# Performance work log

Hardware: AMD Instinct MI355X
Metric: run time of the kernel (lower is better)

Reference implementation:

```python
import jax, jax.numpy as jnp
import numpy as np

N_NODES = 100000
N_EDGES = 1600000
NEG_SLOPE = 0.01  # F.leaky_relu default


def _param(key, shape, scale=0.05):
    return jax.random.normal(key, shape, dtype=jnp.float32) * scale


def setup_inputs() -> dict:
    key = jax.random.key(0)
    ks = jax.random.split(key, 32)
    inp = {
        "x": jax.random.normal(ks[0], (N_NODES, 64), dtype=jnp.float32),
        "edge_index": jax.random.randint(ks[1], (2, N_EDGES), 0, N_NODES, dtype=jnp.int64),
        # encoder SAGEConv params: lin_l (neighbors, with bias) + lin_r (root)
        "ggn1_Wl": _param(ks[2], (128, 64)), "ggn1_b": jnp.zeros((128,), jnp.float32), "ggn1_Wr": _param(ks[3], (128, 64)),
        "ggn2_Wl": _param(ks[4], (128, 128)), "ggn2_b": jnp.zeros((128,), jnp.float32), "ggn2_Wr": _param(ks[5], (128, 128)),
        "ggn3_Wl": _param(ks[6], (128, 128)), "ggn3_b": jnp.zeros((128,), jnp.float32), "ggn3_Wr": _param(ks[7], (128, 128)),
        "tr2_W": _param(ks[8], (64, 128)), "tr2_b": jnp.zeros((64,), jnp.float32),
        # decoder
        "dec1_W": _param(ks[9], (128, 64)), "dec1_b": jnp.zeros((128,), jnp.float32),
        "dec2_Wl": _param(ks[10], (128, 128)), "dec2_b": jnp.zeros((128,), jnp.float32), "dec2_Wr": _param(ks[11], (128, 128)),
        "dec3_Wl": _param(ks[12], (64, 128)), "dec3_b": jnp.zeros((64,), jnp.float32), "dec3_Wr": _param(ks[13], (64, 128)),
        "dec4_Wl": _param(ks[14], (3, 64)), "dec4_b": jnp.zeros((3,), jnp.float32), "dec4_Wr": _param(ks[15], (3, 64)),
    }
    return inp


def _sage(x, src, dst, Wl, b, Wr, n):
    # PyG SAGEConv (aggr='mean'): lin_l(mean_{j->i} x_j) + lin_r(x_i)
    msgs = x[src]                                              # [E, d] gather
    s = jax.ops.segment_sum(msgs, dst, num_segments=n)          # [N, d]
    cnt = jax.ops.segment_sum(jnp.ones((src.shape[0], 1), x.dtype), dst, num_segments=n)
    mean = s / jnp.maximum(cnt, 1.0)
    return mean @ Wl.T + b + x @ Wr.T


def _leaky(h):
    return jnp.where(h > 0, h, NEG_SLOPE * h)


def reference(x, edge_index,
              ggn1_Wl, ggn1_b, ggn1_Wr,
              ggn2_Wl, ggn2_b, ggn2_Wr,
              ggn3_Wl, ggn3_b, ggn3_Wr,
              tr2_W, tr2_b,
              dec1_W, dec1_b,
              dec2_Wl, dec2_b, dec2_Wr,
              dec3_Wl, dec3_b, dec3_Wr,
              dec4_Wl, dec4_b, dec4_Wr):
    n = x.shape[0]
    src, dst = edge_index[0], edge_index[1]  # source_to_target flow
    # --- encode (dropout = identity, deterministic reference) ---
    h = jnp.tanh(_sage(x, src, dst, ggn1_Wl, ggn1_b, ggn1_Wr, n))
    h = jnp.tanh(_sage(h, src, dst, ggn2_Wl, ggn2_b, ggn2_Wr, n))
    h = jnp.tanh(_sage(h, src, dst, ggn3_Wl, ggn3_b, ggn3_Wr, n))
    mu = h @ tr2_W.T + tr2_b
    logvar = mu  # module applies the same tr2 twice
    z = mu       # reparametrize in eval mode returns mu
    # --- decode ---
    o = _leaky(z @ dec1_W.T + dec1_b)
    o = _leaky(_sage(o, src, dst, dec2_Wl, dec2_b, dec2_Wr, n))
    o = jnp.tanh(_sage(o, src, dst, dec3_Wl, dec3_b, dec3_Wr, n))
    z2 = _sage(o, src, dst, dec4_Wl, dec4_b, dec4_Wr, n)
    return (z2[:, :2], z2[:, 2], mu, logvar)
```

## Files before the change

### kernel.cpp

```cpp
#include <hip/hip_runtime.h>
#include <cmath>


constexpr int ACT_NONE = 0, ACT_TANH = 1, ACT_LEAKY = 2;
constexpr int SCAN_CHUNK = 4096;

typedef __attribute__((ext_vector_type(8))) __bf16 bf16x8;
typedef __attribute__((ext_vector_type(4))) float f32x4;
typedef __attribute__((ext_vector_type(4))) unsigned short u16x4;

__device__ __forceinline__ unsigned short f2h(float x) {
  _Float16 h = (_Float16)x;
  unsigned short u;
  __builtin_memcpy(&u, &h, 2);
  return u;
}
__device__ __forceinline__ float hlo(unsigned int u) {
  unsigned short s = (unsigned short)(u & 0xffffu);
  _Float16 h;
  __builtin_memcpy(&h, &s, 2);
  return (float)h;
}
__device__ __forceinline__ float hhi(unsigned int u) {
  unsigned short s = (unsigned short)(u >> 16);
  _Float16 h;
  __builtin_memcpy(&h, &s, 2);
  return (float)h;
}
__device__ __forceinline__ void split_bf16(float x, __bf16& h, __bf16& l) {
  h = (__bf16)x;
  l = (__bf16)(x - (float)h);
}
__device__ __forceinline__ unsigned short b2u(__bf16 b) {
  unsigned short u;
  __builtin_memcpy(&u, &b, 2);
  return u;
}

__global__ __launch_bounds__(256) void split_x_kernel(const float* __restrict__ in,
                                                      __bf16* __restrict__ hi,
                                                      __bf16* __restrict__ lo, int total) {
  int i = (blockIdx.x * 256 + threadIdx.x) * 4;
  if (i >= total) return;
  float4 v = *(const float4*)(in + i);
  float vv[4] = {v.x, v.y, v.z, v.w};
  u16x4 h, l;
#pragma unroll
  for (int j = 0; j < 4; ++j) {
    __bf16 hb, lb;
    split_bf16(vv[j], hb, lb);
    h[j] = b2u(hb);
    l[j] = b2u(lb);
  }
  *(u16x4*)(hi + i) = h;
  *(u16x4*)(lo + i) = l;
}

__global__ __launch_bounds__(256) void split_w_kernel(
    const float* p0, const float* p1, const float* p2, const float* p3,
    const float* p4, const float* p5, const float* p6, const float* p7,
    const float* p8, const float* p9, const float* p10, const float* p11,
    __bf16* __restrict__ hi, __bf16* __restrict__ lo) {
  int b = blockIdx.x;
  const float* src;
  int boff, doff;
  if      (b < 8)   { src = p0;  boff = b;       doff = 0; }
  else if (b < 16)  { src = p1;  boff = b - 8;   doff = 8192; }
  else if (b < 32)  { src = p2;  boff = b - 16;  doff = 16384; }
  else if (b < 48)  { src = p3;  boff = b - 32;  doff = 32768; }
  else if (b < 64)  { src = p4;  boff = b - 48;  doff = 49152; }
  else if (b < 80)  { src = p5;  boff = b - 64;  doff = 65536; }
  else if (b < 88)  { src = p6;  boff = b - 80;  doff = 81920; }
  else if (b < 96)  { src = p7;  boff = b - 88;  doff = 90112; }
  else if (b < 112) { src = p8;  boff = b - 96;  doff = 98304; }
  else if (b < 128) { src = p9;  boff = b - 112; doff = 114688; }
  else if (b < 136) { src = p10; boff = b - 128; doff = 131072; }
  else              { src = p11; boff = b - 136; doff = 139264; }
  int i = boff * 1024 + threadIdx.x * 4;
  float4 v = *(const float4*)(src + i);
  float vv[4] = {v.x, v.y, v.z, v.w};
  u16x4 h, l;
#pragma unroll
  for (int j = 0; j < 4; ++j) {
    __bf16 hb, lb;
    split_bf16(vv[j], hb, lb);
    h[j] = b2u(hb);
    l[j] = b2u(lb);
  }
  *(u16x4*)(hi + doff + i) = h;
  *(u16x4*)(lo + doff + i) = l;
}

__global__ __launch_bounds__(256) void count_rank_kernel(const int* __restrict__ dst,
                                                         int* __restrict__ cnt,
                                                         int* __restrict__ rank, int E) {
  int e = blockIdx.x * 256 + threadIdx.x;
  if (e < E) rank[e] = atomicAdd(&cnt[dst[e]], 1);
}

__global__ __launch_bounds__(1024) void scan_blk_kernel(const int* __restrict__ cnt,
                                                        int* __restrict__ rowptr,
                                                        float* __restrict__ inv,
                                                        int* __restrict__ bsum, int n) {
  __shared__ int wsum[17];
  const int lane = threadIdx.x & 63;
  const int wid = threadIdx.x >> 6;
  const int i0 = blockIdx.x * SCAN_CHUNK + threadIdx.x * 4;
  int v[4];
  if (i0 + 3 < n) {
    int4 t = *(const int4*)(cnt + i0);
    v[0] = t.x; v[1] = t.y; v[2] = t.z; v[3] = t.w;
  } else {
#pragma unroll
    for (int j = 0; j < 4; ++j) v[j] = (i0 + j < n) ? cnt[i0 + j] : 0;
  }
#pragma unroll
  for (int j = 0; j < 4; ++j)
    if (i0 + j < n) inv[i0 + j] = 1.0f / (float)(v[j] > 1 ? v[j] : 1);
  const int s = v[0] + v[1] + v[2] + v[3];
  int x = s;
#pragma unroll
  for (int off = 1; off < 64; off <<= 1) {
    int t = __shfl_up(x, off);
    if (lane >= off) x += t;
  }
  if (lane == 63) wsum[wid + 1] = x;
  __syncthreads();
  if (threadIdx.x == 0) {
    wsum[0] = 0;
    for (int w = 1; w <= 16; ++w) wsum[w] += wsum[w - 1];
    bsum[blockIdx.x] = wsum[16];
  }
  __syncthreads();
  int p = wsum[wid] + x - s;
#pragma unroll
  for (int j = 0; j < 4; ++j) {
    if (i0 + j < n) rowptr[i0 + j] = p;
    p += v[j];
  }
}

__global__ __launch_bounds__(1024) void scan_sums_kernel(int* __restrict__ bsum,
                                                         int* __restrict__ rowptr,
                                                         int nb, int n) {
  __shared__ int wsum[17];
  const int lane = threadIdx.x & 63;
  const int wid = threadIdx.x >> 6;
  const int v = (threadIdx.x < nb) ? bsum[threadIdx.x] : 0;
  int x = v;
#pragma unroll
  for (int off = 1; off < 64; off <<= 1) {
    int t = __shfl_up(x, off);
    if (lane >= off) x += t;
  }
  if (lane == 63) wsum[wid + 1] = x;
  __syncthreads();
  if (threadIdx.x == 0) {
    wsum[0] = 0;
    for (int w = 1; w <= 16; ++w) wsum[w] += wsum[w - 1];
    rowptr[n] = wsum[16];
  }
  __syncthreads();
  if (threadIdx.x < nb) bsum[threadIdx.x] = wsum[wid] + x - v;
}

__global__ __launch_bounds__(1024) void scan_add_kernel(int* __restrict__ rowptr,
                                                        const int* __restrict__ bsum,
                                                        int n) {
  const int off = bsum[blockIdx.x];
  const int i0 = blockIdx.x * SCAN_CHUNK + threadIdx.x * 4;
  if (i0 + 3 < n) {
    int4 t = *(const int4*)(rowptr + i0);
    t.x += off; t.y += off; t.z += off; t.w += off;
    *(int4*)(rowptr + i0) = t;
  } else {
    for (int j = 0; j < 4; ++j)
      if (i0 + j < n) rowptr[i0 + j] += off;
  }
}

__global__ __launch_bounds__(256) void scatter_kernel(const int* __restrict__ src,
                                                      const int* __restrict__ dst,
                                                      const int* __restrict__ rowptr,
                                                      const int* __restrict__ rank,
                                                      int* __restrict__ esrc, int E) {
  int e = blockIdx.x * 256 + threadIdx.x;
  if (e < E) esrc[rowptr[dst[e]] + rank[e]] = src[e];
}

__global__ __launch_bounds__(256) void gather_f32s_kernel(
    const float* __restrict__ in, const int* __restrict__ esrc,
    const int* __restrict__ rowptr, const float* __restrict__ inv,
    __bf16* __restrict__ Mhi, __bf16* __restrict__ Mlo, int n) {
  const int node = blockIdx.x * 4 + (threadIdx.x >> 6);
  const int lane = threadIdx.x & 63;
  if (node >= n) return;
  const int beg = rowptr[node];
  const int end = rowptr[node + 1];
  const float iv = inv[node];
  float a0 = 0.f, a1 = 0.f, a2 = 0.f, a3 = 0.f;
  for (int b = beg; b < end; b += 64) {
    int m = end - b;
    if (m > 64) m = 64;
    int myi = (lane < m) ? esrc[b + lane] : 0;
    int s = 0;
    for (; s + 4 <= m; s += 4) {
      int i0 = __shfl(myi, s);
      int i1 = __shfl(myi, s + 1);
      int i2 = __shfl(myi, s + 2);
      int i3 = __shfl(myi, s + 3);
      a0 += in[(size_t)i0 * 64 + lane];
      a1 += in[(size_t)i1 * 64 + lane];
      a2 += in[(size_t)i2 * 64 + lane];
      a3 += in[(size_t)i3 * 64 + lane];
    }
    for (; s < m; ++s) {
      int i0 = __shfl(myi, s);
      a0 += in[(size_t)i0 * 64 + lane];
    }
  }
  float mv = ((a0 + a1) + (a2 + a3)) * iv;
  __bf16 h, l;
  split_bf16(mv, h, l);
  Mhi[(size_t)node * 64 + lane] = h;
  Mlo[(size_t)node * 64 + lane] = l;
}

__global__ __launch_bounds__(256) void gather_s16_kernel(
    const unsigned short* __restrict__ inq, const int* __restrict__ esrc,
    const int* __restrict__ rowptr, const float* __restrict__ inv,
    __bf16* __restrict__ Mhi, __bf16* __restrict__ Mlo, int n) {
  const int node = blockIdx.x * 4 + (threadIdx.x >> 6);
  const int lane = threadIdx.x & 63;
  if (node >= n) return;
  const int beg = rowptr[node];
  const int end = rowptr[node + 1];
  const float iv = inv[node] * (1.0f / 32767.0f);
  const unsigned int* bu = (const unsigned int*)inq;
  int a0l = 0, a0h = 0, a1l = 0, a1h = 0;
  int a2l = 0, a2h = 0, a3l = 0, a3h = 0;
  for (int b = beg; b < end; b += 64) {
    int m = end - b;
    if (m > 64) m = 64;
    int myi = (lane < m) ? esrc[b + lane] : 0;
    int s = 0;
    for (; s + 4 <= m; s += 4) {
      int i0 = __shfl(myi, s);
      int i1 = __shfl(myi, s + 1);
      int i2 = __shfl(myi, s + 2);
      int i3 = __shfl(myi, s + 3);
      unsigned int u0 = bu[(size_t)i0 * 64 + lane];
      unsigned int u1 = bu[(size_t)i1 * 64 + lane];
      unsigned int u2 = bu[(size_t)i2 * 64 + lane];
      unsigned int u3 = bu[(size_t)i3 * 64 + lane];
      a0l += (int)(short)u0; a0h += ((int)u0) >> 16;
      a1l += (int)(short)u1; a1h += ((int)u1) >> 16;
      a2l += (int)(short)u2; a2h += ((int)u2) >> 16;
      a3l += (int)(short)u3; a3h += ((int)u3) >> 16;
    }
    for (; s < m; ++s) {
      int i0 = __shfl(myi, s);
      unsigned int u0 = bu[(size_t)i0 * 64 + lane];
      a0l += (int)(short)u0; a0h += ((int)u0) >> 16;
    }
  }
  float rx = (float)((a0l + a1l) + (a2l + a3l)) * iv;
  float ry = (float)((a0h + a1h) + (a2h + a3h)) * iv;
  __bf16 h0, l0, h1, l1;
  split_bf16(rx, h0, l0);
  split_bf16(ry, h1, l1);
  ((unsigned int*)Mhi)[(size_t)node * 64 + lane] =
      (unsigned int)b2u(h0) | ((unsigned int)b2u(h1) << 16);
  ((unsigned int*)Mlo)[(size_t)node * 64 + lane] =
      (unsigned int)b2u(l0) | ((unsigned int)b2u(l1) << 16);
}

__global__ __launch_bounds__(256) void gather_h128_kernel(
    const unsigned short* __restrict__ inh, const int* __restrict__ esrc,
    const int* __restrict__ rowptr, const float* __restrict__ inv,
    __bf16* __restrict__ Mhi, __bf16* __restrict__ Mlo, int n) {
  const int node = blockIdx.x * 4 + (threadIdx.x >> 6);
  const int lane = threadIdx.x & 63;
  if (node >= n) return;
  const int beg = rowptr[node];
  const int end = rowptr[node + 1];
  const float iv = inv[node];
  const unsigned int* bu = (const unsigned int*)inh;
  float a0x = 0.f, a0y = 0.f, a1x = 0.f, a1y = 0.f;
  float a2x = 0.f, a2y = 0.f, a3x = 0.f, a3y = 0.f;
  for (int b = beg; b < end; b += 64) {
    int m = end - b;
    if (m > 64) m = 64;
    int myi = (lane < m) ? esrc[b + lane] : 0;
    int s = 0;
    for (; s + 4 <= m; s += 4) {
      int i0 = __shfl(myi, s);
      int i1 = __shfl(myi, s + 1);
      int i2 = __shfl(myi, s + 2);
      int i3 = __shfl(myi, s + 3);
      unsigned int u0 = bu[(size_t)i0 * 64 + lane];
      unsigned int u1 = bu[(size_t)i1 * 64 + lane];
      unsigned int u2 = bu[(size_t)i2 * 64 + lane];
      unsigned int u3 = bu[(size_t)i3 * 64 + lane];
      a0x += hlo(u0); a0y += hhi(u0);
      a1x += hlo(u1); a1y += hhi(u1);
      a2x += hlo(u2); a2y += hhi(u2);
      a3x += hlo(u3); a3y += hhi(u3);
    }
    for (; s < m; ++s) {
      int i0 = __shfl(myi, s);
      unsigned int u0 = bu[(size_t)i0 * 64 + lane];
      a0x += hlo(u0); a0y += hhi(u0);
    }
  }
  float rx = ((a0x + a1x) + (a2x + a3x)) * iv;
  float ry = ((a0y + a1y) + (a2y + a3y)) * iv;
  __bf16 h0, l0, h1, l1;
  split_bf16(rx, h0, l0);
  split_bf16(ry, h1, l1);
  ((unsigned int*)Mhi)[(size_t)node * 64 + lane] =
      (unsigned int)b2u(h0) | ((unsigned int)b2u(h1) << 16);
  ((unsigned int*)Mlo)[(size_t)node * 64 + lane] =
      (unsigned int)b2u(l0) | ((unsigned int)b2u(l1) << 16);
}

__global__ __launch_bounds__(256) void gather_h64_kernel(
    const unsigned short* __restrict__ inh, const int* __restrict__ esrc,
    const int* __restrict__ rowptr, const float* __restrict__ inv,
    float* __restrict__ meanb, int n) {
  const int node = blockIdx.x * 4 + (threadIdx.x >> 6);
  const int lane = threadIdx.x & 63;
  if (node >= n) return;
  const int beg = rowptr[node];
  const int end = rowptr[node + 1];
  const float iv = inv[node];
  const unsigned int* bu = (const unsigned int*)inh;
  const int half = lane >> 5;
  const int hl = lane & 31;
  float ax = 0.f, ay = 0.f, bx = 0.f, by = 0.f;
  for (int b = beg; b < end; b += 64) {
    int m = end - b;
    if (m > 64) m = 64;
    int myi = (lane < m) ? esrc[b + lane] : 0;
    int s = 0;
    for (; s + 4 <= m; s += 4) {
      int i0 = __shfl(myi, s + half);
      int i1 = __shfl(myi, s + 2 + half);
      unsigned int u0 = bu[(size_t)i0 * 32 + hl];
      unsigned int u1 = bu[(size_t)i1 * 32 + hl];
      ax += hlo(u0); ay += hhi(u0);
      bx += hlo(u1); by += hhi(u1);
    }
    for (; s < m; s += 2) {
      int t = s + half;
      if (t < m) {
        int i0 = __shfl(myi, t);
        unsigned int u0 = bu[(size_t)i0 * 32 + hl];
        ax += hlo(u0); ay += hhi(u0);
      }
    }
  }
  float sx = ax + bx, sy = ay + by;
  sx += __shfl_xor(sx, 32);
  sy += __shfl_xor(sy, 32);
  if (half == 0)
    ((float2*)meanb)[(size_t)node * 32 + hl] = make_float2(sx * iv, sy * iv);
}

__global__ __launch_bounds__(256) void gather_mean4_kernel(
    const float* __restrict__ y4, const int* __restrict__ esrc,
    const int* __restrict__ rowptr, const float* __restrict__ inv,
    float* __restrict__ mean4, int n) {
  int i = blockIdx.x * 256 + threadIdx.x;
  if (i >= n) return;
  const int beg = rowptr[i], end = rowptr[i + 1];
  const float iv = inv[i];
  float sx = 0.f, sy = 0.f, sz = 0.f;
  const float4* b = (const float4*)y4;
  for (int j = beg; j < end; ++j) {
    float4 v = b[esrc[j]];
    sx += v.x; sy += v.y; sz += v.z;
  }
  ((float4*)mean4)[i] = make_float4(sx * iv, sy * iv, sz * iv, 0.f);
}

template <int DI, int DO, int ACT, bool AGG, bool ADDMEAN, bool BIAS, int SH, bool OSPLIT>
__global__ __launch_bounds__(256) void node_mfma_kernel(
    const __bf16* __restrict__ Ahi, const __bf16* __restrict__ Alo,
    const __bf16* __restrict__ Mhi, const __bf16* __restrict__ Mlo,
    const __bf16* __restrict__ Wrhi, const __bf16* __restrict__ Wrlo,
    const __bf16* __restrict__ Wlhi, const __bf16* __restrict__ Wllo,
    const float* __restrict__ bias, const float* __restrict__ meanF,
    float* __restrict__ out, float* __restrict__ out2,
    unsigned short* __restrict__ outh,
    __bf16* __restrict__ ohi, __bf16* __restrict__ olo, int n) {
  constexpr int BM = 128;
  constexpr int KC = 32;
  constexpr int KS = 40;
  constexpr int CT = DO / 16;
  __shared__ __align__(16) __bf16 As_hi[BM * KS];
  __shared__ __align__(16) __bf16 As_lo[BM * KS];
  __shared__ __align__(16) __bf16 Ws_hi[DO * KS];
  __shared__ __align__(16) __bf16 Ws_lo[DO * KS];

  const int wv = threadIdx.x >> 6;
  const int lane = threadIdx.x & 63;
  const int lm = lane & 15;
  const int lq = lane >> 4;
  const int row0 = blockIdx.x * BM;

  f32x4 acc[2][CT];
#pragma unroll
  for (int rt = 0; rt < 2; ++rt)
#pragma unroll
    for (int ct = 0; ct < CT; ++ct) acc[rt][ct] = (f32x4){0.f, 0.f, 0.f, 0.f};

  const int nphase = AGG ? 2 : 1;
  for (int phase = 0; phase < nphase; ++phase) {
    const __bf16* AH = (phase == 0) ? Ahi : Mhi;
    const __bf16* AL = (phase == 0) ? Alo : Mlo;
    const __bf16* WH = (phase == 0) ? Wrhi : Wlhi;
    const __bf16* WL = (phase == 0) ? Wrlo : Wllo;
    for (int k0 = 0; k0 < DI; k0 += KC) {
      {
        const int r = threadIdx.x >> 1;
        const int kb = (threadIdx.x & 1) * 16;
        const int row = row0 + r;
        bf16x8 h0, h1, l0, l1;
        if (row < n) {
          const bf16x8* ph = (const bf16x8*)(AH + (size_t)row * DI + k0 + kb);
          const bf16x8* pl = (const bf16x8*)(AL + (size_t)row * DI + k0 + kb);
          h0 = ph[0]; h1 = ph[1];
          l0 = pl[0]; l1 = pl[1];
        } else {
          bf16x8 z;
#pragma unroll
          for (int j = 0; j < 8; ++j) z[j] = (__bf16)0.f;
          h0 = h1 = l0 = l1 = z;
        }
        *(bf16x8*)(&As_hi[r * KS + kb]) = h0;
        *(bf16x8*)(&As_hi[r * KS + kb + 8]) = h1;
        *(bf16x8*)(&As_lo[r * KS + kb]) = l0;
        *(bf16x8*)(&As_lo[r * KS + kb + 8]) = l1;
      }
      if constexpr (DO == 128) {
        const int c = threadIdx.x >> 1;
        const int kb = (threadIdx.x & 1) * 16;
        const bf16x8* ph = (const bf16x8*)(WH + (size_t)c * DI + k0 + kb);
        const bf16x8* pl = (const bf16x8*)(WL + (size_t)c * DI + k0 + kb);
        *(bf16x8*)(&Ws_hi[c * KS + kb]) = ph[0];
        *(bf16x8*)(&Ws_hi[c * KS + kb + 8]) = ph[1];
        *(bf16x8*)(&Ws_lo[c * KS + kb]) = pl[0];
        *(bf16x8*)(&Ws_lo[c * KS + kb + 8]) = pl[1];
      } else {
        const int c = threadIdx.x >> 2;
        const int kb = (threadIdx.x & 3) * 8;
        *(bf16x8*)(&Ws_hi[c * KS + kb]) =
            *(const bf16x8*)(WH + (size_t)c * DI + k0 + kb);
        *(bf16x8*)(&Ws_lo[c * KS + kb]) =
            *(const bf16x8*)(WL + (size_t)c * DI + k0 + kb);
      }
      __syncthreads();
      const int kb = lq * 8;
      bf16x8 ah[2], al[2];
#pragma unroll
      for (int rt = 0; rt < 2; ++rt) {
        const int r = wv * 32 + rt * 16 + lm;
        ah[rt] = *(const bf16x8*)(&As_hi[r * KS + kb]);
        al[rt] = *(const bf16x8*)(&As_lo[r * KS + kb]);
      }
#pragma unroll
      for (int ct = 0; ct < CT; ++ct) {
        const int c = ct * 16 + lm;
        bf16x8 bh = *(const bf16x8*)(&Ws_hi[c * KS + kb]);
        bf16x8 bl = *(const bf16x8*)(&Ws_lo[c * KS + kb]);
#pragma unroll
        for (int rt = 0; rt < 2; ++rt) {
          acc[rt][ct] = __builtin_amdgcn_mfma_f32_16x16x32_bf16(ah[rt], bh, acc[rt][ct], 0, 0, 0);
          acc[rt][ct] = __builtin_amdgcn_mfma_f32_16x16x32_bf16(al[rt], bh, acc[rt][ct], 0, 0, 0);
          acc[rt][ct] = __builtin_amdgcn_mfma_f32_16x16x32_bf16(ah[rt], bl, acc[rt][ct], 0, 0, 0);
        }
      }
      __syncthreads();
    }
  }

#pragma unroll
  for (int rt = 0; rt < 2; ++rt)
#pragma unroll
    for (int ct = 0; ct < CT; ++ct) {
      const int col = ct * 16 + lm;
      const float bval = BIAS ? bias[col] : 0.f;
      f32x4 a = acc[rt][ct];
#pragma unroll
      for (int r = 0; r < 4; ++r) {
        const int row = row0 + wv * 32 + rt * 16 + lq * 4 + r;
        if (row < n) {
          float t = a[r] + bval;
          if (ADDMEAN) t += meanF[(size_t)row * DO + col];
          if (ACT == ACT_TANH) t = tanhf(t);
          else if (ACT == ACT_LEAKY) t = (t > 0.f) ? t : 0.01f * t;
          if (out) out[(size_t)row * DO + col] = t;
          if (out2) out2[(size_t)row * DO + col] = t;
          if constexpr (SH == 1) {
            if (outh) outh[(size_t)row * DO + col] = f2h(t);
          } else if constexpr (SH == 2) {
            if (outh)
              outh[(size_t)row * DO + col] =
                  (unsigned short)(short)__builtin_rintf(t * 32767.0f);
          }
          if constexpr (OSPLIT) {
            __bf16 hb, lb;
            split_bf16(t, hb, lb);
            ohi[(size_t)row * DO + col] = hb;
            olo[(size_t)row * DO + col] = lb;
          }
        }
      }
    }
}

__global__ __launch_bounds__(256) void dec4_pre_kernel(
    const float* __restrict__ hB, const float* __restrict__ Wl,
    float* __restrict__ y4, int n) {
  const int node = blockIdx.x * 4 + (threadIdx.x >> 6);
  const int lane = threadIdx.x & 63;
  if (node >= n) return;
  float v = hB[(size_t)node * 64 + lane];
  float p0 = v * Wl[lane];
  float p1 = v * Wl[64 + lane];
  float p2 = v * Wl[128 + lane];
#pragma unroll
  for (int off = 32; off >= 1; off >>= 1) {
    p0 += __shfl_xor(p0, off);
    p1 += __shfl_xor(p1, off);
    p2 += __shfl_xor(p2, off);
  }
  if (lane == 0) ((float4*)y4)[node] = make_float4(p0, p1, p2, 0.f);
}

__global__ __launch_bounds__(256) void dec4_final_kernel(
    const float* __restrict__ hB, const float* __restrict__ mean4,
    const float* __restrict__ Wr, const float* __restrict__ bias,
    float* __restrict__ out, int n) {
  const int node = blockIdx.x * 4 + (threadIdx.x >> 6);
  const int lane = threadIdx.x & 63;
  if (node >= n) return;
  float v = hB[(size_t)node * 64 + lane];
  float p0 = v * Wr[lane];
  float p1 = v * Wr[64 + lane];
  float p2 = v * Wr[128 + lane];
#pragma unroll
  for (int off = 32; off >= 1; off >>= 1) {
    p0 += __shfl_xor(p0, off);
    p1 += __shfl_xor(p1, off);
    p2 += __shfl_xor(p2, off);
  }
  if (lane == 0) {
    float4 m = ((const float4*)mean4)[node];
    out[2 * (size_t)node]     = p0 + m.x + bias[0];
    out[2 * (size_t)node + 1] = p1 + m.y + bias[1];
    out[2 * (size_t)n + node] = p2 + m.z + bias[2];
  }
}

extern "C" void kernel_launch(void* const* d_in, const int* in_sizes, int n_in,
                              void* d_out, int out_size, void* d_ws, size_t ws_size,
                              hipStream_t stream) {
  const float* x = (const float*)d_in[0];
  const int* ei = (const int*)d_in[1];
  const int N = in_sizes[0] / 64;
  const int E = in_sizes[1] / 2;
  const int* src = ei;
  const int* dst = ei + E;
  const float* g1Wl = (const float*)d_in[2];
  const float* g1b  = (const float*)d_in[3];
  const float* g1Wr = (const float*)d_in[4];
  const float* g2Wl = (const float*)d_in[5];
  const float* g2b  = (const float*)d_in[6];
  const float* g2Wr = (const float*)d_in[7];
  const float* g3Wl = (const float*)d_in[8];
  const float* g3b  = (const float*)d_in[9];
  const float* g3Wr = (const float*)d_in[10];
  const float* t2W  = (const float*)d_in[11];
  const float* t2b  = (const float*)d_in[12];
  const float* d1W  = (const float*)d_in[13];
  const float* d1b  = (const float*)d_in[14];
  const float* d2Wl = (const float*)d_in[15];
  const float* d2b  = (const float*)d_in[16];
  const float* d2Wr = (const float*)d_in[17];
  const float* d3Wl = (const float*)d_in[18];
  const float* d3b  = (const float*)d_in[19];
  const float* d3Wr = (const float*)d_in[20];
  const float* d4Wl = (const float*)d_in[21];
  const float* d4b  = (const float*)d_in[22];
  const float* d4Wr = (const float*)d_in[23];

  const size_t N64 = (size_t)N * 64;
  const size_t N128 = (size_t)N * 128;

  char* w = (char*)d_ws;
  auto alloc = [&](size_t bytes) {
    char* p = w;
    w += (bytes + 255) & ~(size_t)255;
    return p;
  };
  __bf16* Ahi = (__bf16*)alloc(N128 * 2);
  __bf16* Alo = (__bf16*)alloc(N128 * 2);
  __bf16* Bhi = (__bf16*)alloc(N128 * 2);
  __bf16* Blo = (__bf16*)alloc(N128 * 2);
  float*  meanF = (float*)alloc(N128 * 4);
  __bf16* xhi = (__bf16*)alloc(N64 * 2);
  __bf16* xlo = (__bf16*)alloc(N64 * 2);
  __bf16* Whi = (__bf16*)alloc(147456 * 2);
  __bf16* Wlo = (__bf16*)alloc(147456 * 2);
  int*    cnt = (int*)alloc((size_t)N * 4);
  float*  inv = (float*)alloc((size_t)N * 4);
  int*    rowp = (int*)alloc(((size_t)N + 1) * 4);
  int*    rank = (int*)alloc((size_t)E * 4);
  int*    esrc = (int*)alloc((size_t)E * 4);
  unsigned short* shB = (unsigned short*)alloc(N128 * 2);

  __bf16* Mhi = (__bf16*)meanF;
  __bf16* Mlo = Mhi + N128;
  int*    bsum = (int*)meanF;
  float*  y4 = meanF;
  float*  mean4 = meanF + 4 * (size_t)N;
  float*  hBf = meanF + N64;
  __bf16* muhi = xhi;
  __bf16* mulo = xlo;
  unsigned short* shC = (unsigned short*)xhi;

  float* out = (float*)d_out;
  float* mu  = out + 3 * (size_t)N;
  float* lv  = mu + 64 * (size_t)N;

  const int NB = (N + 127) / 128;
  const int GB = (N + 3) / 4;
  const int SB = (N + SCAN_CHUNK - 1) / SCAN_CHUNK;

  const __bf16 *W_g1Wl_h = Whi + 0,      *W_g1Wl_l = Wlo + 0;
  const __bf16 *W_g1Wr_h = Whi + 8192,   *W_g1Wr_l = Wlo + 8192;
  const __bf16 *W_g2Wl_h = Whi + 16384,  *W_g2Wl_l = Wlo + 16384;
  const __bf16 *W_g2Wr_h = Whi + 32768,  *W_g2Wr_l = Wlo + 32768;
  const __bf16 *W_g3Wl_h = Whi + 49152,  *W_g3Wl_l = Wlo + 49152;
  const __bf16 *W_g3Wr_h = Whi + 65536,  *W_g3Wr_l = Wlo + 65536;
  const __bf16 *W_t2W_h  = Whi + 81920,  *W_t2W_l  = Wlo + 81920;
  const __bf16 *W_d1W_h  = Whi + 90112,  *W_d1W_l  = Wlo + 90112;
  const __bf16 *W_d2Wl_h = Whi + 98304,  *W_d2Wl_l = Wlo + 98304;
  const __bf16 *W_d2Wr_h = Whi + 114688, *W_d2Wr_l = Wlo + 114688;
  const __bf16 *W_d3Wl_h = Whi + 131072, *W_d3Wl_l = Wlo + 131072;
  const __bf16 *W_d3Wr_h = Whi + 139264, *W_d3Wr_l = Wlo + 139264;

  split_x_kernel<<<(int)((N64 + 1023) / 1024), 256, 0, stream>>>(x, xhi, xlo, (int)N64);
  split_w_kernel<<<144, 256, 0, stream>>>(g1Wl, g1Wr, g2Wl, g2Wr, g3Wl, g3Wr,
                                          t2W, d1W, d2Wl, d2Wr, d3Wl, d3Wr, Whi, Wlo);

  hipMemsetAsync(cnt, 0, (size_t)N * sizeof(int), stream);
  count_rank_kernel<<<(E + 255) / 256, 256, 0, stream>>>(dst, cnt, rank, E);
  scan_blk_kernel<<<SB, 1024, 0, stream>>>(cnt, rowp, inv, bsum, N);
  scan_sums_kernel<<<1, 1024, 0, stream>>>(bsum, rowp, SB, N);
  scan_add_kernel<<<SB, 1024, 0, stream>>>(rowp, bsum, N);
  scatter_kernel<<<(E + 255) / 256, 256, 0, stream>>>(src, dst, rowp, rank, esrc, E);

  gather_f32s_kernel<<<GB, 256, 0, stream>>>(x, esrc, rowp, inv, Mhi, Mlo, N);
  node_mfma_kernel<64, 128, ACT_TANH, true, false, true, 2, true><<<NB, 256, 0, stream>>>(
      xhi, xlo, Mhi, Mlo, W_g1Wr_h, W_g1Wr_l, W_g1Wl_h, W_g1Wl_l, g1b, nullptr,
      nullptr, nullptr, shB, Ahi, Alo, N);

  gather_s16_kernel<<<GB, 256, 0, stream>>>(shB, esrc, rowp, inv, Mhi, Mlo, N);
  node_mfma_kernel<128, 128, ACT_TANH, true, false, true, 2, true><<<NB, 256, 0, stream>>>(
      Ahi, Alo, Mhi, Mlo, W_g2Wr_h, W_g2Wr_l, W_g2Wl_h, W_g2Wl_l, g2b, nullptr,
      nullptr, nullptr, shB, Bhi, Blo, N);

  gather_s16_kernel<<<GB, 256, 0, stream>>>(shB, esrc, rowp, inv, Mhi, Mlo, N);
  node_mfma_kernel<128, 128, ACT_TANH, true, false, true, 0, true><<<NB, 256, 0, stream>>>(
      Bhi, Blo, Mhi, Mlo, W_g3Wr_h, W_g3Wr_l, W_g3Wl_h, W_g3Wl_l, g3b, nullptr,
      nullptr, nullptr, nullptr, Ahi, Alo, N);

  node_mfma_kernel<128, 64, ACT_NONE, false, false, true, 0, true><<<NB, 256, 0, stream>>>(
      Ahi, Alo, nullptr, nullptr, W_t2W_h, W_t2W_l, nullptr, nullptr, t2b, nullptr,
      mu, lv, nullptr, muhi, mulo, N);

  node_mfma_kernel<64, 128, ACT_LEAKY, false, false, true, 1, true><<<NB, 256, 0, stream>>>(
      muhi, mulo, nullptr, nullptr, W_d1W_h, W_d1W_l, nullptr, nullptr, d1b, nullptr,
      nullptr, nullptr, shB, Bhi, Blo, N);

  gather_h128_kernel<<<GB, 256, 0, stream>>>(shB, esrc, rowp, inv, Mhi, Mlo, N);
  node_mfma_kernel<128, 128, ACT_LEAKY, true, false, true, 0, true><<<NB, 256, 0, stream>>>(
      Bhi, Blo, Mhi, Mlo, W_d2Wr_h, W_d2Wr_l, W_d2Wl_h, W_d2Wl_l, d2b, nullptr,
      nullptr, nullptr, nullptr, Ahi, Alo, N);

  node_mfma_kernel<128, 64, ACT_NONE, false, false, false, 1, false><<<NB, 256, 0, stream>>>(
      Ahi, Alo, nullptr, nullptr, W_d3Wl_h, W_d3Wl_l, nullptr, nullptr, nullptr, nullptr,
      nullptr, nullptr, shC, nullptr, nullptr, N);
  gather_h64_kernel<<<GB, 256, 0, stream>>>(shC, esrc, rowp, inv, meanF, N);
  node_mfma_kernel<128, 64, ACT_TANH, false, true, true, 0, false><<<NB, 256, 0, stream>>>(
      Ahi, Alo, nullptr, nullptr, W_d3Wr_h, W_d3Wr_l, nullptr, nullptr, d3b, meanF,
      hBf, nullptr, nullptr, nullptr, nullptr, N);

  dec4_pre_kernel<<<GB, 256, 0, stream>>>(hBf, d4Wl, y4, N);
  gather_mean4_kernel<<<(N + 255) / 256, 256, 0, stream>>>(y4, esrc, rowp, inv, mean4, N);
  dec4_final_kernel<<<GB, 256, 0, stream>>>(hBf, mean4, d4Wr, d4b, out, N);
}
```

Measured before the change: 998.1 us.

## Load MFMA operands directly from global memory, dropping LDS staging and barriers

The node GEMM kernel no longer stages A and W tiles through shared memory. Each lane now loads its MFMA fragments straight from global memory (weights through cache), which removes both __syncthreads per K-chunk and the LDS round trip. In exchange, weight fragments are reloaded by every wave from L1/L2, and the A-row loads become strided per lane rather than coalesced, so global load efficiency may drop.

```diff
diff --git a/kernel.cpp b/kernel.cpp
--- a/kernel.cpp
+++ b/kernel.cpp
@@ -396,12 +396,7 @@
     __bf16* __restrict__ ohi, __bf16* __restrict__ olo, int n) {
   constexpr int BM = 128;
   constexpr int KC = 32;
-  constexpr int KS = 40;
   constexpr int CT = DO / 16;
-  __shared__ __align__(16) __bf16 As_hi[BM * KS];
-  __shared__ __align__(16) __bf16 As_lo[BM * KS];
-  __shared__ __align__(16) __bf16 Ws_hi[DO * KS];
-  __shared__ __align__(16) __bf16 Ws_lo[DO * KS];
 
   const int wv = threadIdx.x >> 6;
   const int lane = threadIdx.x & 63;
@@ -414,6 +409,16 @@
   for (int rt = 0; rt < 2; ++rt)
 #pragma unroll
     for (int ct = 0; ct < CT; ++ct) acc[rt][ct] = (f32x4){0.f, 0.f, 0.f, 0.f};
+
+  bf16x8 zf;
+#pragma unroll
+  for (int j = 0; j < 8; ++j) zf[j] = (__bf16)0.f;
+
+  const int rA0 = row0 + wv * 32 + lm;
+  const int rA1 = rA0 + 16;
+  const bool ok0 = rA0 < n;
+  const bool ok1 = rA1 < n;
+  const int kofs = lq * 8;
 
   const int nphase = AGG ? 2 : 1;
   for (int phase = 0; phase < nphase; ++phase) {
@@ -421,59 +426,23 @@
     const __bf16* AL = (phase == 0) ? Alo : Mlo;
     const __bf16* WH = (phase == 0) ? Wrhi : Wlhi;
     const __bf16* WL = (phase == 0) ? Wrlo : Wllo;
+    const __bf16* pA0h = AH + (size_t)rA0 * DI + kofs;
+    const __bf16* pA0l = AL + (size_t)rA0 * DI + kofs;
+    const __bf16* pA1h = AH + (size_t)rA1 * DI + kofs;
+    const __bf16* pA1l = AL + (size_t)rA1 * DI + kofs;
+    const __bf16* pWh = WH + (size_t)lm * DI + kofs;
+    const __bf16* pWl = WL + (size_t)lm * DI + kofs;
+#pragma unroll 1
     for (int k0 = 0; k0 < DI; k0 += KC) {
-      {
-        const int r = threadIdx.x >> 1;
-        const int kb = (threadIdx.x & 1) * 16;
-        const int row = row0 + r;
-        bf16x8 h0, h1, l0, l1;
-        if (row < n) {
-          const bf16x8* ph = (const bf16x8*)(AH + (size_t)row * DI + k0 + kb);
-          const bf16x8* pl = (const bf16x8*)(AL + (size_t)row * DI + k0 + kb);
-          h0 = ph[0]; h1 = ph[1];
-          l0 = pl[0]; l1 = pl[1];
-        } else {
-          bf16x8 z;
-#pragma unroll
-          for (int j = 0; j < 8; ++j) z[j] = (__bf16)0.f;
-          h0 = h1 = l0 = l1 = z;
-        }
-        *(bf16x8*)(&As_hi[r * KS + kb]) = h0;
-        *(bf16x8*)(&As_hi[r * KS + kb + 8]) = h1;
-        *(bf16x8*)(&As_lo[r * KS + kb]) = l0;
-        *(bf16x8*)(&As_lo[r * KS + kb + 8]) = l1;
-      }
-      if constexpr (DO == 128) {
-        const int c = threadIdx.x >> 1;
-        const int kb = (threadIdx.x & 1) * 16;
-        const bf16x8* ph = (const bf16x8*)(WH + (size_t)c * DI + k0 + kb);
-        const bf16x8* pl = (const bf16x8*)(WL + (size_t)c * DI + k0 + kb);
-        *(bf16x8*)(&Ws_hi[c * KS + kb]) = ph[0];
-        *(bf16x8*)(&Ws_hi[c * KS + kb + 8]) = ph[1];
-        *(bf16x8*)(&Ws_lo[c * KS + kb]) = pl[0];
-        *(bf16x8*)(&Ws_lo[c * KS + kb + 8]) = pl[1];
-      } else {
-        const int c = threadIdx.x >> 2;
-        const int kb = (threadIdx.x & 3) * 8;
-        *(bf16x8*)(&Ws_hi[c * KS + kb]) =
-            *(const bf16x8*)(WH + (size_t)c * DI + k0 + kb);
-        *(bf16x8*)(&Ws_lo[c * KS + kb]) =
-            *(const bf16x8*)(WL + (size_t)c * DI + k0 + kb);
-      }
-      __syncthreads();
-      const int kb = lq * 8;
       bf16x8 ah[2], al[2];
-#pragma unroll
-      for (int rt = 0; rt < 2; ++rt) {
-        const int r = wv * 32 + rt * 16 + lm;
-        ah[rt] = *(const bf16x8*)(&As_hi[r * KS + kb]);
-        al[rt] = *(const bf16x8*)(&As_lo[r * KS + kb]);
-      }
+      ah[0] = ok0 ? *(const bf16x8*)(pA0h + k0) : zf;
+      al[0] = ok0 ? *(const bf16x8*)(pA0l + k0) : zf;
+      ah[1] = ok1 ? *(const bf16x8*)(pA1h + k0) : zf;
+      al[1] = ok1 ? *(const bf16x8*)(pA1l + k0) : zf;
 #pragma unroll
       for (int ct = 0; ct < CT; ++ct) {
-        const int c = ct * 16 + lm;
-        bf16x8 bh = *(const bf16x8*)(&Ws_hi[c * KS + kb]);
-        bf16x8 bl = *(const bf16x8*)(&Ws_lo[c * KS + kb]);
+        bf16x8 bh = *(const bf16x8*)(pWh + (size_t)ct * 16 * DI + k0);
+        bf16x8 bl = *(const bf16x8*)(pWl + (size_t)ct * 16 * DI + k0);
 #pragma unroll
         for (int rt = 0; rt < 2; ++rt) {
           acc[rt][ct] = __builtin_amdgcn_mfma_f32_16x16x32_bf16(ah[rt], bh, acc[rt][ct], 0, 0, 0);
@@ -481,7 +450,6 @@
           acc[rt][ct] = __builtin_amdgcn_mfma_f32_16x16x32_bf16(ah[rt], bl, acc[rt][ct], 0, 0, 0);
         }
       }
-      __syncthreads();
     }
   }
 
```

After: 1.213 ms. 1.22x slower.
